# Kernel tuning notes

Hardware: AMD Instinct MI355X
Metric: run time of the kernel (lower is better)

The kernel has to match this reference:

```python
import jax, jax.numpy as jnp
import numpy as np

STAGES = [80, 40, 20]
INPUT = 640
NUM_CLASSES = 80
B = 32
PRE_NMS = 1000      # top-k candidates fed to NMS (fixed-shape surrogate for full sort)
MAX_DET = 100       # max_num_detections
IOU_TH = 0.5
CLASS_OFF = 4096.0  # batched_nms trick: offset boxes per class so classes never overlap


def setup_inputs() -> dict:
    key = jax.random.key(0)
    ks = jax.random.split(key, 6)
    inp = {}
    for i, s in enumerate(STAGES):
        inp[f"cls{i}"] = jax.random.normal(ks[2 * i], (B, NUM_CLASSES, s, s), dtype=jnp.float32)
        # positive ltrb distances, up to ~64 px
        inp[f"box{i}"] = jax.random.uniform(ks[2 * i + 1], (B, 4, s, s), dtype=jnp.float32) * 64.0
    return inp


def _decode_level(cls, box, stage):
    # cls: [B,C,H,W], box: [B,4,H,W]
    step = INPUT // stage
    cls = jax.nn.sigmoid(jnp.transpose(cls, (0, 2, 3, 1)))   # [B,H,W,C]
    conf = jnp.max(cls, axis=-1)                             # [B,H,W]
    cidx = jnp.argmax(cls, axis=-1)                          # [B,H,W]
    box = jnp.transpose(box, (0, 2, 3, 1))                   # [B,H,W,4]
    grid = jnp.arange(stage, dtype=box.dtype) * step
    gx, gy = jnp.meshgrid(grid, grid, indexing='xy')
    block = jnp.stack([gx, gy], axis=-1)                     # [H,W,2]
    xy1 = block - box[..., :2]
    xy2 = block + box[..., 2:4]
    boxes = jnp.concatenate([xy1, xy2], axis=-1).reshape(box.shape[0], -1, 4)
    return boxes, conf.reshape(conf.shape[0], -1), cidx.reshape(cidx.shape[0], -1)


def _iou_matrix(b):
    # b: [N,4] -> [N,N] pairwise IoU
    area = jnp.maximum(b[:, 2] - b[:, 0], 0.) * jnp.maximum(b[:, 3] - b[:, 1], 0.)
    lt = jnp.maximum(b[:, None, :2], b[None, :, :2])
    rb = jnp.minimum(b[:, None, 2:], b[None, :, 2:])
    wh = jnp.maximum(rb - lt, 0.)
    inter = wh[..., 0] * wh[..., 1]
    return inter / (area[:, None] + area[None, :] - inter + 1e-7)


def _nms_image(boxes, scores, classes):
    # class-aware (batched) NMS via per-class coordinate offset
    off = classes.astype(boxes.dtype) * CLASS_OFF
    ob = boxes + off[:, None]
    s_top, idx = jax.lax.top_k(scores, PRE_NMS)
    b_top = ob[idx]                                          # [PRE,4], score-sorted desc
    iou = _iou_matrix(b_top)
    ar = jnp.arange(PRE_NMS)

    def body(i, supp):
        row = (iou[i] > IOU_TH) & (ar > i)
        return jnp.where(supp[i], supp, supp | row)

    supp = jax.lax.fori_loop(0, PRE_NMS, body, jnp.zeros((PRE_NMS,), bool))
    kept_scores = jnp.where(supp, -jnp.inf, s_top)
    sel_s, sel = jax.lax.top_k(kept_scores, MAX_DET)
    final = idx[sel]                                         # indices into original 8400
    valid = jnp.isfinite(sel_s)
    out_b = jnp.where(valid[:, None], boxes[final], 0.)
    out_s = jnp.where(valid, scores[final], 0.)
    out_c = jnp.where(valid, classes[final], -1)
    return out_b, out_s, out_c


def reference(cls0, box0, cls1, box1, cls2, box2):
    parts = [_decode_level(c, b, s) for c, b, s in
             zip([cls0, cls1, cls2], [box0, box1, box2], STAGES)]
    boxes = jnp.concatenate([p[0] for p in parts], axis=1)    # [B,8400,4]
    scores = jnp.concatenate([p[1] for p in parts], axis=1)   # [B,8400]
    classes = jnp.concatenate([p[2] for p in parts], axis=1)  # [B,8400]
    ob, os_, oc = jax.vmap(_nms_image)(boxes, scores, classes)
    boxes_with_scores = jnp.concatenate([ob, os_[..., None]], axis=-1)  # [B,MAX_DET,5]
    return boxes_with_scores, oc
```

## Files before the change

kernel.cpp:

```cpp
#include <hip/hip_runtime.h>

typedef unsigned int u32;
typedef unsigned long long u64;

#define NB 32
#define NCLS 80
#define NANCHOR 8400
#define PRE 1000
#define MAXDET 100
#define NT 1024

__global__ __launch_bounds__(256) void decode_kernel(
        const float* __restrict__ cls0, const float* __restrict__ box0,
        const float* __restrict__ cls1, const float* __restrict__ box1,
        const float* __restrict__ cls2, const float* __restrict__ box2,
        float* __restrict__ ws_scores, float4* __restrict__ ws_boxes,
        int* __restrict__ ws_cls) {
    const int NQ = NANCHOR / 4;
    const int lane = threadIdx.x & 63;
    const int wv = threadIdx.x >> 6;
    const int q = blockIdx.x * 64 + lane;
    int b = q / NQ;
    int r = (q - b * NQ) * 4;

    const float* cp; const float* bp;
    int HW, hw, rowlen, step;
    if (r < 6400) {
        cp = cls0 + (size_t)b * NCLS * 6400; bp = box0 + (size_t)b * 4 * 6400;
        HW = 6400; hw = r;        rowlen = 80; step = 8;
    } else if (r < 8000) {
        cp = cls1 + (size_t)b * NCLS * 1600; bp = box1 + (size_t)b * 4 * 1600;
        HW = 1600; hw = r - 6400; rowlen = 40; step = 16;
    } else {
        cp = cls2 + (size_t)b * NCLS * 400;  bp = box2 + (size_t)b * 4 * 400;
        HW = 400;  hw = r - 8000; rowlen = 20; step = 32;
    }

    __shared__ float s_m[4][4][64];
    __shared__ int   s_c[4][4][64];

    {
        const float* cps = cp + (size_t)(wv * 20) * HW + hw;
        float4 m = *(const float4*)cps;
        int c0 = wv * 20, c1 = c0, c2 = c0, c3 = c0;
#pragma unroll
        for (int c = 1; c < 20; ++c) {
            float4 v = *(const float4*)(cps + (size_t)c * HW);
            int cc = wv * 20 + c;
            if (v.x > m.x) { m.x = v.x; c0 = cc; }
            if (v.y > m.y) { m.y = v.y; c1 = cc; }
            if (v.z > m.z) { m.z = v.z; c2 = cc; }
            if (v.w > m.w) { m.w = v.w; c3 = cc; }
        }
        s_m[wv][0][lane] = m.x; s_c[wv][0][lane] = c0;
        s_m[wv][1][lane] = m.y; s_c[wv][1][lane] = c1;
        s_m[wv][2][lane] = m.z; s_c[wv][2][lane] = c2;
        s_m[wv][3][lane] = m.w; s_c[wv][3][lane] = c3;
    }
    __syncthreads();

    if (wv == 0) {
        float mm[4]; int cc[4];
#pragma unroll
        for (int j = 0; j < 4; ++j) {
            float mv = s_m[0][j][lane]; int cv = s_c[0][j][lane];
#pragma unroll
            for (int s = 1; s < 4; ++s) {
                float v = s_m[s][j][lane];
                if (v > mv) { mv = v; cv = s_c[s][j][lane]; }
            }
            mm[j] = mv; cc[j] = cv;
        }

        float4 L  = *(const float4*)(bp + hw);
        float4 T  = *(const float4*)(bp + HW + hw);
        float4 R  = *(const float4*)(bp + 2 * HW + hw);
        float4 Bo = *(const float4*)(bp + 3 * HW + hw);

        int h = hw / rowlen, w = hw - h * rowlen;
        float gy  = (float)(h * step);
        float gx0 = (float)(w * step);
        float gx1 = gx0 + (float)step;
        float gx2 = gx1 + (float)step;
        float gx3 = gx2 + (float)step;

        int g = b * NANCHOR + r;
        float4 sc;
        sc.x = 1.0f / (1.0f + expf(-mm[0]));
        sc.y = 1.0f / (1.0f + expf(-mm[1]));
        sc.z = 1.0f / (1.0f + expf(-mm[2]));
        sc.w = 1.0f / (1.0f + expf(-mm[3]));
        *(float4*)(ws_scores + g) = sc;
        ws_boxes[g + 0] = make_float4(gx0 - L.x, gy - T.x, gx0 + R.x, gy + Bo.x);
        ws_boxes[g + 1] = make_float4(gx1 - L.y, gy - T.y, gx1 + R.y, gy + Bo.y);
        ws_boxes[g + 2] = make_float4(gx2 - L.z, gy - T.z, gx2 + R.z, gy + Bo.z);
        ws_boxes[g + 3] = make_float4(gx3 - L.w, gy - T.w, gx3 + R.w, gy + Bo.w);
        *(int4*)(ws_cls + g) = make_int4(cc[0], cc[1], cc[2], cc[3]);
    }
}

__device__ __forceinline__ u64 shfl_xor_u64(u64 v, int m) {
    u32 lo = (u32)v, hi = (u32)(v >> 32);
    lo = (u32)__shfl_xor((int)lo, m, 64);
    hi = (u32)__shfl_xor((int)hi, m, 64);
    return ((u64)hi << 32) | (u64)lo;
}

__device__ __forceinline__ u64 readlane_u64(u64 v, int l) {
    u32 lo = (u32)v, hi = (u32)(v >> 32);
    lo = (u32)__builtin_amdgcn_readlane((int)lo, l);
    hi = (u32)__builtin_amdgcn_readlane((int)hi, l);
    return ((u64)hi << 32) | (u64)lo;
}

__device__ __forceinline__ void suffix_scan_1024(int* sh, int* swsum, int* swadd) {
    const int tid = threadIdx.x, lane = tid & 63, wv = tid >> 6;
    int s = sh[tid];
#pragma unroll
    for (int off = 1; off < 64; off <<= 1) {
        int u = __shfl_down(s, off, 64);
        if (lane + off < 64) s += u;
    }
    if (lane == 0) swsum[wv] = s;
    __syncthreads();
    if (tid < 64) {
        int t = (lane < 16) ? swsum[lane] : 0;
#pragma unroll
        for (int off = 1; off < 16; off <<= 1) {
            int u = __shfl_down(t, off, 64);
            if (lane + off < 64) t += u;
        }
        int ab = __shfl_down(t, 1, 64);
        if (lane < 16) swadd[lane] = (lane == 15) ? 0 : ab;
    }
    __syncthreads();
    sh[tid] = s + swadd[wv];
    __syncthreads();
}

__global__ __launch_bounds__(NT) void select_sort_kernel(
        const float* __restrict__ ws_scores, const float4* __restrict__ ws_boxes,
        const int* __restrict__ ws_cls, u64* __restrict__ ws_keys,
        float* __restrict__ ws_sx1, float* __restrict__ ws_sy1,
        float* __restrict__ ws_sx2, float* __restrict__ ws_sy2,
        float* __restrict__ ws_sar) {
    const int b = blockIdx.x;
    const int tid = threadIdx.x;

    __shared__ int s_hist[1024];
    __shared__ u64 s_key[2048];
    __shared__ int s_wsum[16], s_wadd[16];
    __shared__ int s_C, s_base, s_cnt;
    __shared__ u32 s_thresh;

    const float* sc = ws_scores + (size_t)b * NANCHOR;

    s_hist[tid] = 0;
    s_key[tid] = 0ULL;
    s_key[tid + 1024] = 0ULL;
    if (tid == 0) s_cnt = 0;
    __syncthreads();

    u32 sb[9];
#pragma unroll
    for (int k = 0; k < 9; ++k) {
        int a = tid + k * NT;
        if (a < NANCHOR) {
            u32 x = __float_as_uint(sc[a]);
            sb[k] = x;
            atomicAdd(&s_hist[x >> 20], 1);
        } else sb[k] = 0;
    }
    __syncthreads();
    suffix_scan_1024(s_hist, s_wsum, s_wadd);
    {
        int sfx = s_hist[tid];
        int nxt = (tid < 1023) ? s_hist[tid + 1] : 0;
        if (sfx >= PRE && (tid == 1023 || nxt < PRE)) { s_C = tid; s_base = nxt; }
    }
    __syncthreads();
    const int C = s_C, base = s_base;
    s_hist[tid] = 0;
    __syncthreads();

#pragma unroll
    for (int k = 0; k < 9; ++k) {
        int a = tid + k * NT;
        if (a < NANCHOR && (int)(sb[k] >> 20) == C)
            atomicAdd(&s_hist[(sb[k] >> 10) & 1023], 1);
    }
    __syncthreads();
    suffix_scan_1024(s_hist, s_wsum, s_wadd);
    {
        int sfx = base + s_hist[tid];
        int nxt = base + ((tid < 1023) ? s_hist[tid + 1] : 0);
        if (sfx >= PRE && (tid == 1023 || nxt < PRE))
            s_thresh = ((u32)C << 20) | ((u32)tid << 10);
    }
    __syncthreads();
    const u32 thresh = s_thresh;

#pragma unroll
    for (int k = 0; k < 9; ++k) {
        int a = tid + k * NT;
        if (a < NANCHOR && sb[k] >= thresh) {
            int pos = atomicAdd(&s_cnt, 1);
            if (pos < 2048)
                s_key[pos] = ((u64)sb[k] << 14) | (u64)(NANCHOR - 1 - a);
        }
    }
    __syncthreads();
    const int cnt = s_cnt;

    if (cnt > 1024) {
        bool prevBig = false;
        for (int k = 2; k <= 2048; k <<= 1) {
            for (int j = k >> 1; j > 0; j >>= 1) {
                const bool big = (j >= 64);
                if (big || prevBig) __syncthreads();
                else __builtin_amdgcn_wave_barrier();
                for (int i = tid; i < 2048; i += NT) {
                    int ixj = i ^ j;
                    if (ixj > i) {
                        u64 va = s_key[i], vb = s_key[ixj];
                        bool desc = ((i & k) == 0);
                        if (desc ? (va < vb) : (va > vb)) { s_key[i] = vb; s_key[ixj] = va; }
                    }
                }
                prevBig = big;
            }
        }
        __syncthreads();
    } else {
        if (tid < 64) {
            const int lane = tid;
            u64 v[16];
#pragma unroll
            for (int r = 0; r < 16; ++r) v[r] = s_key[(r << 6) | lane];

#define CE_REG(ra, rb, DESC) { u64 a_ = v[(ra)], b_ = v[(rb)];                        \
            if ((DESC) ? (a_ < b_) : (a_ > b_)) { v[(ra)] = b_; v[(rb)] = a_; } }
#define CE_SHFL(rr_, jj_, DESC) { u64 a_ = v[(rr_)]; u64 p_ = shfl_xor_u64(a_, (jj_)); \
            bool up_ = ((lane & (jj_)) == 0); bool km_ = ((DESC) == up_);              \
            bool pg_ = (p_ > a_); v[(rr_)] = (km_ == pg_) ? p_ : a_; }

#pragma unroll
            for (int kl = 1; kl <= 10; ++kl) {
                const int K = 1 << kl;
#pragma unroll
                for (int js = 10; js >= 0; --js) {
                    if (js > kl - 1) continue;
                    const int j = 1 << js;
                    if (j >= 64) {
                        const int jr = j >> 6;
#pragma unroll
                        for (int r = 0; r < 16; ++r) {
                            if ((r & jr) == 0) {
                                const bool desc = ((r & (K >> 6)) == 0);
                                CE_REG(r, r | jr, desc);
                            }
                        }
                    } else {
#pragma unroll
                        for (int r = 0; r < 16; ++r) {
                            if (K >= 64) {
                                const bool desc = ((r & (K >> 6)) == 0);
                                CE_SHFL(r, j, desc);
                            } else {
                                CE_SHFL(r, j, ((lane & K) == 0));
                            }
                        }
                    }
                }
            }
#undef CE_REG
#undef CE_SHFL

#pragma unroll
            for (int r = 0; r < 16; ++r) s_key[(r << 6) | lane] = v[r];
        }
        __syncthreads();
    }

    {
        u64 key = s_key[tid];
        ws_keys[(b << 10) + tid] = key;
        int idx = (NANCHOR - 1) - (int)(key & 16383ULL);
        float4 bx = ws_boxes[(size_t)b * NANCHOR + idx];
        int c = ws_cls[(size_t)b * NANCHOR + idx];
        float off = (float)c * 4096.0f;
        float x1 = bx.x + off, y1 = bx.y + off, x2 = bx.z + off, y2 = bx.w + off;
        int o = (b << 10) + tid;
        ws_sx1[o] = x1; ws_sy1[o] = y1; ws_sx2[o] = x2; ws_sy2[o] = y2;
        ws_sar[o] = fmaxf(x2 - x1, 0.0f) * fmaxf(y2 - y1, 0.0f);
    }
}

__global__ __launch_bounds__(1024) void iou_bits_kernel(
        const float* __restrict__ ws_sx1, const float* __restrict__ ws_sy1,
        const float* __restrict__ ws_sx2, const float* __restrict__ ws_sy2,
        const float* __restrict__ ws_sar,
        u64* __restrict__ ws_bits, u64* __restrict__ ws_diag) {
    const int blk = blockIdx.x;
    const int b = blk >> 4, tile = blk & 15;
    const int tid = threadIdx.x;

    __shared__ float sx1[1024], sy1[1024], sx2[1024], sy2[1024], sar[1024];
    {
        int o = (b << 10) + tid;
        sx1[tid] = ws_sx1[o]; sy1[tid] = ws_sy1[o];
        sx2[tid] = ws_sx2[o]; sy2[tid] = ws_sy2[o];
        sar[tid] = ws_sar[o];
    }
    __syncthreads();

    const int rl = tid & 63, w = tid >> 6;
    const int r = (tile << 6) + rl;
    u64 bits = 0ULL;
    if (r < 1000 && w >= tile) {
        float xi1 = sx1[r], yi1 = sy1[r], xi2 = sx2[r], yi2 = sy2[r], ai = sar[r];
        const int jbase = w << 6;
#pragma unroll 8
        for (int kb = 0; kb < 64; ++kb) {
            int j = jbase + kb;
            float lx = fmaxf(xi1, sx1[j]);
            float ly = fmaxf(yi1, sy1[j]);
            float rx = fminf(xi2, sx2[j]);
            float ry = fminf(yi2, sy2[j]);
            float wx = fmaxf(rx - lx, 0.0f);
            float wy = fmaxf(ry - ly, 0.0f);
            float inter = wx * wy;
            float iou = inter / (ai + sar[j] - inter + 1e-7f);
            bits |= (iou > 0.5f) ? (1ULL << kb) : 0ULL;
        }
        u64 mlow;
        if (w == tile) {
            int bpos = r & 63;
            mlow = (bpos == 63) ? 0ULL : (~0ULL << (bpos + 1));
        } else mlow = ~0ULL;
        u64 mhigh = (jbase + 64 <= 1000) ? ~0ULL : ((1ULL << (1000 - jbase)) - 1ULL);
        bits &= mlow & mhigh;
    }
    ws_bits[((size_t)b << 14) + ((size_t)r << 4) + w] = bits;
    if (w == tile) ws_diag[(b << 10) + r] = bits;
}

__global__ __launch_bounds__(128) void nms_scan_kernel(
        const u64* __restrict__ ws_bits, const u64* __restrict__ ws_diag,
        const u64* __restrict__ ws_keys, const float4* __restrict__ ws_boxes,
        const int* __restrict__ ws_cls, float* __restrict__ out) {
    const int b = blockIdx.x;
    const int tid = threadIdx.x;

    __shared__ int s_keep[MAXDET];
    __shared__ int s_nk;

    if (tid < 64) {
        const int lane = tid;
        const u64* bits = ws_bits + ((size_t)b << 14);
        const u64* diag = ws_diag + ((size_t)b << 10);
        int nkept = 0;
        for (int wi = 0; wi < 16 && nkept < MAXDET; ++wi) {
            const int wbase = wi << 6;
            u64 acc = 0ULL;
            if (lane < nkept)       acc  = bits[((size_t)s_keep[lane] << 4) + wi];
            if (lane + 64 < nkept)  acc |= bits[((size_t)s_keep[lane + 64] << 4) + wi];
#pragma unroll
            for (int off = 32; off > 0; off >>= 1) acc |= shfl_xor_u64(acc, off);
            u64 cur = acc;
            u64 rw = diag[wbase + lane];
            const int nb = (wbase + 64 <= 1000) ? 64 : (1000 - wbase);
            for (int bit = 0; bit < nb; ++bit) {
                if (!((cur >> bit) & 1ULL)) {
                    if (lane == 0) s_keep[nkept] = wbase + bit;
                    nkept++;
                    if (nkept >= MAXDET) break;
                    cur |= readlane_u64(rw, bit);
                }
            }
        }
        if (lane == 0) s_nk = nkept;
    }
    __syncthreads();

    const int nk = s_nk;
    if (tid < MAXDET) {
        float* o = out + ((size_t)b * MAXDET + tid) * 5;
        float* oc = out + (size_t)NB * MAXDET * 5 + (size_t)b * MAXDET + tid;
        if (tid < nk) {
            int rank = s_keep[tid];
            u64 key = ws_keys[(b << 10) + rank];
            int idx = (NANCHOR - 1) - (int)(key & 16383ULL);
            float score = __uint_as_float((u32)(key >> 14));
            float4 bx = ws_boxes[(size_t)b * NANCHOR + idx];
            int c = ws_cls[(size_t)b * NANCHOR + idx];
            o[0] = bx.x; o[1] = bx.y; o[2] = bx.z; o[3] = bx.w; o[4] = score;
            *oc = (float)c;
        } else {
            o[0] = 0.0f; o[1] = 0.0f; o[2] = 0.0f; o[3] = 0.0f; o[4] = 0.0f;
            *oc = -1.0f;
        }
    }
}

extern "C" void kernel_launch(void* const* d_in, const int* in_sizes, int n_in,
                              void* d_out, int out_size, void* d_ws, size_t ws_size,
                              hipStream_t stream) {
    const float* cls0 = (const float*)d_in[0];
    const float* box0 = (const float*)d_in[1];
    const float* cls1 = (const float*)d_in[2];
    const float* box1 = (const float*)d_in[3];
    const float* cls2 = (const float*)d_in[4];
    const float* box2 = (const float*)d_in[5];

    float* ws = (float*)d_ws;
    float* ws_scores = ws;
    float4* ws_boxes = (float4*)(ws + NB * NANCHOR);
    int* ws_cls = (int*)(ws + (size_t)NB * NANCHOR * 5);
    float* base6 = ws + (size_t)NB * NANCHOR * 6;
    u64* ws_keys = (u64*)base6;
    float* ws_sx1 = base6 + 65536;
    float* ws_sy1 = ws_sx1 + NB * 1024;
    float* ws_sx2 = ws_sy1 + NB * 1024;
    float* ws_sy2 = ws_sx2 + NB * 1024;
    float* ws_sar = ws_sy2 + NB * 1024;
    u64* ws_bits = (u64*)(ws_sar + NB * 1024);
    u64* ws_diag = ws_bits + (size_t)NB * 1024 * 16;

    int nquads = NB * (NANCHOR / 4);
    decode_kernel<<<nquads / 64, 256, 0, stream>>>(
        cls0, box0, cls1, box1, cls2, box2, ws_scores, ws_boxes, ws_cls);

    select_sort_kernel<<<NB, NT, 0, stream>>>(ws_scores, ws_boxes, ws_cls, ws_keys,
                                              ws_sx1, ws_sy1, ws_sx2, ws_sy2, ws_sar);

    iou_bits_kernel<<<NB * 16, 1024, 0, stream>>>(ws_sx1, ws_sy1, ws_sx2, ws_sy2, ws_sar,
                                                  ws_bits, ws_diag);

    nms_scan_kernel<<<NB, 128, 0, stream>>>(ws_bits, ws_diag, ws_keys, ws_boxes, ws_cls,
                                            (float*)d_out);
}
```

Baseline: 185.7 us.

## Replace single-wave register bitonic sort with block-wide rank sort

When the candidate count fits in 1024, the single-wavefront register bitonic sort is replaced by a counting (rank) sort. Each of the 1024 threads counts how many keys exceed its own key and scatters the key to that position. Slots past the valid count are filled with distinct small keys so ranks stay unique. This uses all threads and LDS broadcast reads instead of one wave doing serial shuffles, at the cost of O(N^2) LDS reads overall.

Measured after the change: 184.3 us. No clear change (-0.7%).

```diff
diff --git a/kernel.cpp b/kernel.cpp
--- a/kernel.cpp
+++ b/kernel.cpp
@@ -232,53 +232,18 @@
         }
         __syncthreads();
     } else {
-        if (tid < 64) {
-            const int lane = tid;
-            u64 v[16];
-#pragma unroll
-            for (int r = 0; r < 16; ++r) v[r] = s_key[(r << 6) | lane];
-
-#define CE_REG(ra, rb, DESC) { u64 a_ = v[(ra)], b_ = v[(rb)];                        \
-            if ((DESC) ? (a_ < b_) : (a_ > b_)) { v[(ra)] = b_; v[(rb)] = a_; } }
-#define CE_SHFL(rr_, jj_, DESC) { u64 a_ = v[(rr_)]; u64 p_ = shfl_xor_u64(a_, (jj_)); \
-            bool up_ = ((lane & (jj_)) == 0); bool km_ = ((DESC) == up_);              \
-            bool pg_ = (p_ > a_); v[(rr_)] = (km_ == pg_) ? p_ : a_; }
-
-#pragma unroll
-            for (int kl = 1; kl <= 10; ++kl) {
-                const int K = 1 << kl;
-#pragma unroll
-                for (int js = 10; js >= 0; --js) {
-                    if (js > kl - 1) continue;
-                    const int j = 1 << js;
-                    if (j >= 64) {
-                        const int jr = j >> 6;
-#pragma unroll
-                        for (int r = 0; r < 16; ++r) {
-                            if ((r & jr) == 0) {
-                                const bool desc = ((r & (K >> 6)) == 0);
-                                CE_REG(r, r | jr, desc);
-                            }
-                        }
-                    } else {
-#pragma unroll
-                        for (int r = 0; r < 16; ++r) {
-                            if (K >= 64) {
-                                const bool desc = ((r & (K >> 6)) == 0);
-                                CE_SHFL(r, j, desc);
-                            } else {
-                                CE_SHFL(r, j, ((lane & K) == 0));
-                            }
-                        }
-                    }
-                }
-            }
-#undef CE_REG
-#undef CE_SHFL
-
-#pragma unroll
-            for (int r = 0; r < 16; ++r) s_key[(r << 6) | lane] = v[r];
-        }
+        if (tid >= cnt) s_key[tid] = (u64)tid;
+        __syncthreads();
+        const u64 my = s_key[tid];
+        int rank = 0;
+#pragma unroll 4
+        for (int j = 0; j < 1024; j += 4) {
+            u64 k0 = s_key[j + 0], k1 = s_key[j + 1];
+            u64 k2 = s_key[j + 2], k3 = s_key[j + 3];
+            rank += (int)(k0 > my) + (int)(k1 > my) + (int)(k2 > my) + (int)(k3 > my);
+        }
+        __syncthreads();
+        s_key[rank] = my;
         __syncthreads();
     }
 
```
